# Optimization experiments

Measured on AMD Instinct MI355X. Metric: run time of the kernel, lower is better.

Reference implementation:

```python
import jax, jax.numpy as jnp
import numpy as np

B, S = 2, 2048
HID = 2560
NH, NKV, HD = 20, 5, 128
GROUPS = NH // NKV  # 4
THETA = 500000.0
RMS_EPS = 1e-6  # RMSNorm default eps used for attn_sub_norm
NEG_INF = -1e9


def pack_ternary(key, M, K):
    """Pack ternary weights {-1,0,1} (stored as trits {0,1,2}) into SIMD
    block-interleaved uint8 layout: per 128-elem block, byte j holds
    weights j+0 (bits 6:7), j+32 (4:5), j+64 (2:3), j+96 (0:1)."""
    t = jax.random.randint(key, (M, K), 0, 3).astype(jnp.uint8)
    t = t.reshape(M, K // 128, 4, 32)
    byte = (t[:, :, 0] << 6) | (t[:, :, 1] << 4) | (t[:, :, 2] << 2) | t[:, :, 3]
    return byte.reshape(M, K // 4)


def unpack_ternary(packed):
    """Inverse of pack_ternary -> float weights in {-1,0,1}. (M, K//4) -> (M, K)."""
    M, Kp = packed.shape
    nb = Kp // 32
    b = packed.reshape(M, nb, 32)
    fields = jnp.stack([(b >> 6) & 3, (b >> 4) & 3, (b >> 2) & 3, b & 3], axis=2)
    return fields.reshape(M, nb * 128).astype(jnp.float32) - 1.0


def bitlinear(x, packed, scale):
    w = unpack_ternary(packed) * scale  # (out, in)
    return jnp.einsum('bsi,oi->bso', x, w)


def rotate_half(x):
    h = x.shape[-1] // 2
    return jnp.concatenate([-x[..., h:], x[..., :h]], axis=-1)


def rms_norm(x, w, eps=RMS_EPS):
    var = jnp.mean(jnp.square(x.astype(jnp.float32)), axis=-1, keepdims=True)
    return (w * (x * jax.lax.rsqrt(var + eps))).astype(x.dtype)


def setup_inputs() -> dict:
    key = jax.random.key(0)
    ks = jax.random.split(key, 6)
    hidden_states = jax.random.normal(ks[0], (B, S, HID), dtype=jnp.float32)
    causal = jnp.tril(jnp.ones((S, S), dtype=bool))
    attention_mask = jnp.where(causal, 0.0, NEG_INF).astype(jnp.float32)[None, None]
    return {
        'hidden_states': hidden_states,
        'attention_mask': attention_mask,
        'q_w': pack_ternary(ks[1], NH * HD, HID),
        'k_w': pack_ternary(ks[2], NKV * HD, HID),
        'v_w': pack_ternary(ks[3], NKV * HD, HID),
        'o_w': pack_ternary(ks[4], HID, NH * HD),
        'q_scale': jnp.float32(0.02),
        'k_scale': jnp.float32(0.02),
        'v_scale': jnp.float32(0.02),
        'o_scale': jnp.float32(0.02),
        'attn_norm_w': jnp.ones((NH * HD,), dtype=jnp.float32),
    }


def reference(hidden_states, attention_mask, q_w, k_w, v_w, o_w,
              q_scale, k_scale, v_scale, o_scale, attn_norm_w):
    bsz, seq_len, _ = hidden_states.shape
    q = bitlinear(hidden_states, q_w, q_scale)
    k = bitlinear(hidden_states, k_w, k_scale)
    v = bitlinear(hidden_states, v_w, v_scale)
    q = q.reshape(bsz, seq_len, NH, HD).transpose(0, 2, 1, 3)    # (b,h,s,d)
    k = k.reshape(bsz, seq_len, NKV, HD).transpose(0, 2, 1, 3)
    v = v.reshape(bsz, seq_len, NKV, HD).transpose(0, 2, 1, 3)
    # rotary embedding
    inv_freq = 1.0 / (THETA ** (jnp.arange(0, HD, 2, dtype=jnp.float32) / HD))
    t = jnp.arange(seq_len, dtype=jnp.float32)
    freqs = t[:, None] * inv_freq[None, :]            # (s, d/2)
    emb = jnp.concatenate([freqs, freqs], axis=-1)    # (s, d)
    cos, sin = jnp.cos(emb), jnp.sin(emb)
    q = q * cos + rotate_half(q) * sin
    k = k * cos + rotate_half(k) * sin
    # GQA: repeat kv heads
    k = jnp.repeat(k, GROUPS, axis=1)
    v = jnp.repeat(v, GROUPS, axis=1)
    scores = jnp.einsum('bhqd,bhkd->bhqk', q, k) / np.sqrt(HD).astype(np.float32)
    scores = scores + attention_mask
    attn = jax.nn.softmax(scores.astype(jnp.float32), axis=-1).astype(q.dtype)
    out = jnp.einsum('bhqk,bhkd->bhqd', attn, v)
    out = out.transpose(0, 2, 1, 3).reshape(bsz, seq_len, NH * HD)
    out = rms_norm(out, attn_norm_w)
    return bitlinear(out, o_w, o_scale)
```

## Files before the change

### kernel.cpp

```cpp
#include <hip/hip_runtime.h>
#include <cstdint>
#include <cstddef>

typedef __bf16 bf16x8 __attribute__((ext_vector_type(8)));
typedef float  f32x4  __attribute__((ext_vector_type(4)));
typedef int    i32x4  __attribute__((ext_vector_type(4)));
typedef unsigned short u16x4 __attribute__((ext_vector_type(4)));

#define DEV __device__ __forceinline__
#define NEGINF (-__builtin_inff())

DEV uint16_t f2bf(float f) {
  union { float f; uint32_t u; } v; v.f = f;
  uint32_t u = v.u;
  u += 0x7FFFu + ((u >> 16) & 1u);
  return (uint16_t)(u >> 16);
}
DEV float bf2f(uint16_t h) {
  union { uint32_t u; float f; } v; v.u = ((uint32_t)h) << 16;
  return v.f;
}

DEV void gload_lds16(const void* g, void* l) {
  __builtin_amdgcn_global_load_lds(
      (const __attribute__((address_space(1))) void*)g,
      (__attribute__((address_space(3))) void*)l, 16, 0, 0);
}


__global__ void k_f32_to_bf16(const float* __restrict__ in, uint16_t* __restrict__ out, int n4) {
  int i = blockIdx.x * blockDim.x + threadIdx.x;
  if (i >= n4) return;
  f32x4 v = *(const f32x4*)(in + (size_t)i * 4);
  u16x4 o;
  o[0] = f2bf(v[0]); o[1] = f2bf(v[1]); o[2] = f2bf(v[2]); o[3] = f2bf(v[3]);
  *(u16x4*)(out + (size_t)i * 4) = o;
}

__global__ void k_unpack(const uint32_t* __restrict__ p, uint16_t* __restrict__ w, int total, int Kq) {
  int idx = blockIdx.x * blockDim.x + threadIdx.x;
  if (idx >= total) return;
  int row = idx / Kq, pc = idx - row * Kq;
  int blk = pc >> 5, j = pc & 31;
  uint32_t b = p[idx] & 0xFFu;
  size_t base = (size_t)row * (size_t)(Kq * 4) + (size_t)blk * 128 + j;
  w[base]      = f2bf((float)((b >> 6) & 3u) - 1.0f);
  w[base + 32] = f2bf((float)((b >> 4) & 3u) - 1.0f);
  w[base + 64] = f2bf((float)((b >> 2) & 3u) - 1.0f);
  w[base + 96] = f2bf((float)(b & 3u) - 1.0f);
}

__global__ void k_rope_table(float* __restrict__ cosT, float* __restrict__ sinT) {
  int idx = blockIdx.x * blockDim.x + threadIdx.x;
  int s = idx >> 6, i = idx & 63;
  float inv = expf((float)i * (-13.122363377404328f / 64.0f));
  float fr = (float)s * inv;
  cosT[idx] = cosf(fr);
  sinT[idx] = sinf(fr);
}

__global__ void k_rope(uint16_t* __restrict__ buf, const float* __restrict__ cosT,
                       const float* __restrict__ sinT, int H, int total) {
  int idx = blockIdx.x * blockDim.x + threadIdx.x;
  if (idx >= total) return;
  int d = idx & 63;
  int t = idx >> 6;
  int h = t % H;
  int row = t / H;
  int s = row & 2047;
  size_t base = (size_t)row * (size_t)(H * 128) + (size_t)h * 128 + d;
  float x1 = bf2f(buf[base]), x2 = bf2f(buf[base + 64]);
  float c = cosT[(s << 6) + d], sn = sinT[(s << 6) + d];
  buf[base]      = f2bf(x1 * c - x2 * sn);
  buf[base + 64] = f2bf(x2 * c + x1 * sn);
}

template<int MODE>
__global__ __launch_bounds__(256, 2)
void k_gemm(const uint16_t* __restrict__ A, const uint16_t* __restrict__ W,
            uint16_t* __restrict__ Qo, uint16_t* __restrict__ Ko, uint16_t* __restrict__ Vo,
            float* __restrict__ Fo,
            const float* __restrict__ s0p, const float* __restrict__ s1p, const float* __restrict__ s2p,
            int M, int N, int K)
{
  __shared__ uint16_t As[128 * 64];
  __shared__ uint16_t Bs[128 * 64];
  const int tid = threadIdx.x;
  const int n0 = blockIdx.x * 128, m0 = blockIdx.y * 128;
  const int lane = tid & 63, w = tid >> 6;
  const int wm = (w >> 1) * 64, wn = (w & 1) * 64;
  const int lr = lane & 15, lg = lane >> 4, lk = lg * 8;
  const size_t K2 = (size_t)K * 2;
  f32x4 acc[4][4] = {};

  const int srow = tid >> 3;
  const int cprime = ((tid & 7) * 16) ^ ((srow & 7) << 4);
  const uint8_t* Ag = (const uint8_t*)A + (size_t)(m0 + srow) * K2 + cprime;
  const uint8_t* Wg = (const uint8_t*)W + (size_t)(n0 + srow) * K2 + cprime;
  char* Al = (char*)As + w * 1024;
  char* Bl = (char*)Bs + w * 1024;

  for (size_t k0b = 0; k0b < K2; k0b += 128) {
    #pragma unroll
    for (int i = 0; i < 4; ++i)
      gload_lds16(Ag + (size_t)(i * 32) * K2 + k0b, Al + i * 4096);
    #pragma unroll
    for (int i = 0; i < 4; ++i)
      gload_lds16(Wg + (size_t)(i * 32) * K2 + k0b, Bl + i * 4096);
    __syncthreads();
    #pragma unroll
    for (int kc = 0; kc < 64; kc += 32) {
      bf16x8 a[4], b[4];
      #pragma unroll
      for (int i = 0; i < 4; ++i) {
        const int r = wm + i * 16 + lr;
        a[i] = *(const bf16x8*)((const char*)As + r * 128 + (((kc + lk) * 2) ^ ((r & 7) << 4)));
      }
      #pragma unroll
      for (int j = 0; j < 4; ++j) {
        const int r = wn + j * 16 + lr;
        b[j] = *(const bf16x8*)((const char*)Bs + r * 128 + (((kc + lk) * 2) ^ ((r & 7) << 4)));
      }
      #pragma unroll
      for (int i = 0; i < 4; ++i)
        #pragma unroll
        for (int j = 0; j < 4; ++j)
          acc[i][j] = __builtin_amdgcn_mfma_f32_16x16x32_bf16(a[i], b[j], acc[i][j], 0, 0, 0);
    }
    __syncthreads();
  }

  if (MODE == 0) {
    const float qs = *s0p, ks = *s1p, vs = *s2p;
    #pragma unroll
    for (int i = 0; i < 4; ++i) {
      const int rowb = m0 + wm + i * 16 + lg * 4;
      #pragma unroll
      for (int j = 0; j < 4; ++j) {
        const int col = n0 + wn + j * 16 + lr;
        #pragma unroll
        for (int r = 0; r < 4; ++r) {
          const int rr = rowb + r;
          const float v = acc[i][j][r];
          if (col < 2560) {
            Qo[(size_t)rr * 2560 + col] = f2bf(v * qs);
          } else if (col < 3200) {
            Ko[(size_t)rr * 640 + (col - 2560)] = f2bf(v * ks);
          } else {
            const int n2 = col - 3200;
            const int kvh = n2 >> 7, d = n2 & 127;
            const int bb = rr >> 11, ss = rr & 2047;
            Vo[(((size_t)(bb * 5 + kvh) * 128 + d) << 11) + ss] = f2bf(v * vs);
          }
        }
      }
    }
  } else {
    const float os = *s0p;
    #pragma unroll
    for (int i = 0; i < 4; ++i) {
      const int rowb = m0 + wm + i * 16 + lg * 4;
      #pragma unroll
      for (int j = 0; j < 4; ++j) {
        const int col = n0 + wn + j * 16 + lr;
        #pragma unroll
        for (int r = 0; r < 4; ++r)
          Fo[(size_t)(rowb + r) * N + col] = acc[i][j][r] * os;
      }
    }
  }
}

__global__ __launch_bounds__(256, 2)
void k_attn(const uint16_t* __restrict__ Q, const uint16_t* __restrict__ Kb,
            const uint16_t* __restrict__ Vt, uint16_t* __restrict__ Ob)
{
  __shared__ char Klds[2][16384];
  __shared__ char Vlds[2][16384];
  __shared__ uint16_t p_lds[4][16][72];

  const int lin = blockIdx.x;
  const int gslot = (lin & 7) * 80 + (lin >> 3);
  const int bk = gslot >> 6;
  const int st = 63 - (gslot & 63);
  const int b = bk / 5, kvh = bk - b * 5;

  const int tid = threadIdx.x, lane = tid & 63, w = tid >> 6;
  const int lr = lane & 15, lg = lane >> 4, lk = lg * 8;
  const int h = kvh * 4 + w;
  uint16_t (*pl)[72] = p_lds[w];
  const int kswz = (lr & 7) << 4;

  const uint8_t* Kg = (const uint8_t*)(Kb + (size_t)b * 2048 * 640 + (size_t)kvh * 128);
  const uint8_t* Vg = (const uint8_t*)(Vt + ((size_t)(b * 5 + kvh) * 128) * 2048);

  const int krow = tid >> 4;
  const int kcol = ((tid & 15) * 16) ^ ((krow & 7) << 4);
  const int vrow = tid >> 3;
  const int vcol = ((tid & 7) * 16) ^ ((vrow & 7) << 4);
  const int dst16 = tid * 16;

  const float C = 0.127531019577f;

  const int q0 = st * 32;
  const int ns = (q0 + 95) >> 6;

  bf16x8 qf0[4], qf1[4];
  {
    const size_t qb0 = ((size_t)(b * 2048 + q0 + lr)) * 2560 + (size_t)h * 128 + lk;
    #pragma unroll
    for (int c = 0; c < 4; ++c) {
      qf0[c] = *(const bf16x8*)&Q[qb0 + c * 32];
      qf1[c] = *(const bf16x8*)&Q[qb0 + 16 * 2560 + c * 32];
    }
  }

  {
    const uint8_t* Ks = Kg + (size_t)krow * 1280 + kcol;
    const uint8_t* Vs = Vg + (size_t)vrow * 4096 + vcol;
    #pragma unroll
    for (int i = 0; i < 4; ++i) gload_lds16(Ks + (size_t)i * 16 * 1280, Klds[0] + dst16 + i * 4096);
    #pragma unroll
    for (int i = 0; i < 4; ++i) gload_lds16(Vs + (size_t)i * 32 * 4096, Vlds[0] + dst16 + i * 4096);
  }

  int cur = 0;
  float m0 = NEGINF, m1 = NEGINF, l0 = 0.f, l1 = 0.f;
  f32x4 oa0[8] = {}, oa1[8] = {};

  #pragma unroll 1
  for (int stp = 0; stp < ns; ++stp) {
    const int k0 = stp * 64;
    __syncthreads();

    if (stp + 1 < ns) {
      const int kn = k0 + 64;
      const uint8_t* Ks = Kg + (size_t)(kn + krow) * 1280 + kcol;
      const uint8_t* Vs = Vg + (size_t)vrow * 4096 + (size_t)kn * 2 + vcol;
      char* Kd = Klds[cur ^ 1] + dst16;
      char* Vd = Vlds[cur ^ 1] + dst16;
      #pragma unroll
      for (int i = 0; i < 4; ++i) gload_lds16(Ks + (size_t)i * 16 * 1280, Kd + i * 4096);
      #pragma unroll
      for (int i = 0; i < 4; ++i) gload_lds16(Vs + (size_t)i * 32 * 4096, Vd + i * 4096);
    }

    const char* Kc = Klds[cur];
    const char* Vc = Vlds[cur];

    __builtin_amdgcn_s_setprio(1);
    f32x4 sa0[4] = {}, sa1[4] = {};
    #pragma unroll
    for (int t = 0; t < 4; ++t) {
      #pragma unroll
      for (int c = 0; c < 4; ++c) {
        bf16x8 kf = *(const bf16x8*)(Kc + (t * 16 + lr) * 256 + ((c * 64 + lg * 16) ^ kswz));
        sa0[t] = __builtin_amdgcn_mfma_f32_16x16x32_bf16(kf, qf0[c], sa0[t], 0, 0, 0);
        sa1[t] = __builtin_amdgcn_mfma_f32_16x16x32_bf16(kf, qf1[c], sa1[t], 0, 0, 0);
      }
    }
    __builtin_amdgcn_s_setprio(0);

    #pragma unroll
    for (int g = 0; g < 2; ++g) {
      const f32x4* sa = g ? sa1 : sa0;
      f32x4* oa = g ? oa1 : oa0;
      float& m = g ? m1 : m0;
      float& l = g ? l1 : l0;
      const int q0g = q0 + 16 * g;

      float u[16];
      if (k0 + 63 > q0g) {
        #pragma unroll
        for (int t = 0; t < 4; ++t)
          #pragma unroll
          for (int r = 0; r < 4; ++r)
            u[t * 4 + r] = (k0 + t * 16 + lg * 4 + r <= q0g + lr) ? sa[t][r] * C : NEGINF;
      } else {
        #pragma unroll
        for (int t = 0; t < 4; ++t)
          #pragma unroll
          for (int r = 0; r < 4; ++r)
            u[t * 4 + r] = sa[t][r] * C;
      }
      float m01 = fmaxf(u[0], u[1]),   m23 = fmaxf(u[2], u[3]);
      float m45 = fmaxf(u[4], u[5]),   m67 = fmaxf(u[6], u[7]);
      float m89 = fmaxf(u[8], u[9]),   mab = fmaxf(u[10], u[11]);
      float mcd = fmaxf(u[12], u[13]), mef = fmaxf(u[14], u[15]);
      float mx = fmaxf(fmaxf(fmaxf(m01, m23), fmaxf(m45, m67)),
                       fmaxf(fmaxf(m89, mab), fmaxf(mcd, mef)));
      mx = fmaxf(mx, __shfl_xor(mx, 16));
      mx = fmaxf(mx, __shfl_xor(mx, 32));
      const float mn = fmaxf(m, mx);
      const float resc = __builtin_exp2f(m - mn);
      m = mn;
      float pv[16];
      #pragma unroll
      for (int i = 0; i < 16; ++i) pv[i] = __builtin_exp2f(u[i] - mn);
      float s0 = (pv[0] + pv[1]) + (pv[2] + pv[3]);
      float s1 = (pv[4] + pv[5]) + (pv[6] + pv[7]);
      float s2 = (pv[8] + pv[9]) + (pv[10] + pv[11]);
      float s3 = (pv[12] + pv[13]) + (pv[14] + pv[15]);
      l = l * resc + ((s0 + s1) + (s2 + s3));
      #pragma unroll
      for (int t = 0; t < 4; ++t) {
        union { __bf16 b4[4]; unsigned long long u64; } pk;
        #pragma unroll
        for (int r = 0; r < 4; ++r) pk.b4[r] = (__bf16)pv[t * 4 + r];
        *(unsigned long long*)&pl[lr][t * 16 + lg * 4] = pk.u64;
      }
      #pragma unroll
      for (int dc = 0; dc < 8; ++dc) {
        oa[dc][0] *= resc; oa[dc][1] *= resc; oa[dc][2] *= resc; oa[dc][3] *= resc;
      }
      bf16x8 pa0 = *(const bf16x8*)&pl[lr][lk];
      bf16x8 pa1 = *(const bf16x8*)&pl[lr][32 + lk];
      __builtin_amdgcn_s_setprio(1);
      #pragma unroll
      for (int dc = 0; dc < 8; ++dc) {
        bf16x8 vf0 = *(const bf16x8*)(Vc + (dc * 16 + lr) * 128 + ((lg * 16) ^ kswz));
        bf16x8 vf1 = *(const bf16x8*)(Vc + (dc * 16 + lr) * 128 + ((64 + lg * 16) ^ kswz));
        oa[dc] = __builtin_amdgcn_mfma_f32_16x16x32_bf16(vf0, pa0, oa[dc], 0, 0, 0);
        oa[dc] = __builtin_amdgcn_mfma_f32_16x16x32_bf16(vf1, pa1, oa[dc], 0, 0, 0);
      }
      __builtin_amdgcn_s_setprio(0);
    }
    cur ^= 1;
  }

  #pragma unroll
  for (int g = 0; g < 2; ++g) {
    f32x4* oa = g ? oa1 : oa0;
    float lf = g ? l1 : l0;
    lf += __shfl_xor(lf, 16);
    lf += __shfl_xor(lf, 32);
    const float inv = 1.0f / lf;
    const size_t obase = ((size_t)(b * 2048 + q0 + 16 * g + lr)) * 2560 + (size_t)h * 128;
    #pragma unroll
    for (int dc = 0; dc < 8; ++dc) {
      union { __bf16 b4[4]; unsigned long long u64; } ok;
      #pragma unroll
      for (int r = 0; r < 4; ++r) ok.b4[r] = (__bf16)(oa[dc][r] * inv);
      *(unsigned long long*)&Ob[obase + dc * 16 + lg * 4] = ok.u64;
    }
  }
}

__global__ __launch_bounds__(256)
void k_rmsnorm(const uint16_t* __restrict__ X, const float* __restrict__ g, uint16_t* __restrict__ Y)
{
  const int row = blockIdx.x;
  const int tid = threadIdx.x;
  const uint16_t* x = X + (size_t)row * 2560;
  float ss = 0.f;
  #pragma unroll
  for (int it = 0; it < 10; ++it) {
    const int i = tid + it * 256;
    const float v = bf2f(x[i]);
    ss += v * v;
  }
  #pragma unroll
  for (int off = 1; off < 64; off <<= 1) ss += __shfl_xor(ss, off, 64);
  __shared__ float sred[4];
  if ((tid & 63) == 0) sred[tid >> 6] = ss;
  __syncthreads();
  const float tot = sred[0] + sred[1] + sred[2] + sred[3];
  const float rs = rsqrtf(tot * (1.0f / 2560.0f) + 1e-6f);
  uint16_t* y = Y + (size_t)row * 2560;
  #pragma unroll
  for (int it = 0; it < 10; ++it) {
    const int i = tid + it * 256;
    y[i] = f2bf(bf2f(x[i]) * rs * g[i]);
  }
}

extern "C" void kernel_launch(void* const* d_in, const int* in_sizes, int n_in,
                              void* d_out, int out_size, void* d_ws, size_t ws_size,
                              hipStream_t stream)
{
  const float*    x     = (const float*)d_in[0];
  const uint32_t* qw    = (const uint32_t*)d_in[2];
  const uint32_t* kw    = (const uint32_t*)d_in[3];
  const uint32_t* vw    = (const uint32_t*)d_in[4];
  const uint32_t* ow    = (const uint32_t*)d_in[5];
  const float*    qs    = (const float*)d_in[6];
  const float*    ks    = (const float*)d_in[7];
  const float*    vs    = (const float*)d_in[8];
  const float*    os    = (const float*)d_in[9];
  const float*    gnorm = (const float*)d_in[10];

  char* ws = (char*)d_ws;
  uint16_t* xb   = (uint16_t*)(ws + 0);
  uint16_t* wqkv = (uint16_t*)(ws + 20971520);
  uint16_t* owb  = (uint16_t*)(ws + 40632320);
  float*    cosT = (float*)   (ws + 53739520);
  float*    sinT = (float*)   (ws + 54263808);
  uint16_t* Qb   = (uint16_t*)(ws + 54788096);
  uint16_t* Kb   = (uint16_t*)(ws + 75759616);
  uint16_t* Vt   = (uint16_t*)(ws + 81002496);

  k_f32_to_bf16<<<10240, 256, 0, stream>>>(x, xb, 2621440);
  k_unpack<<<6400, 256, 0, stream>>>(qw, wqkv, 1638400, 640);
  k_unpack<<<1600, 256, 0, stream>>>(kw, wqkv + (size_t)2560 * 2560, 409600, 640);
  k_unpack<<<1600, 256, 0, stream>>>(vw, wqkv + (size_t)3200 * 2560, 409600, 640);
  k_unpack<<<6400, 256, 0, stream>>>(ow, owb, 1638400, 640);
  k_rope_table<<<512, 256, 0, stream>>>(cosT, sinT);

  k_gemm<0><<<dim3(30, 32), 256, 0, stream>>>(xb, wqkv, Qb, Kb, Vt, nullptr,
                                              qs, ks, vs, 4096, 3840, 2560);
  k_rope<<<20480, 256, 0, stream>>>(Qb, cosT, sinT, 20, 5242880);
  k_rope<<<5120, 256, 0, stream>>>(Kb, cosT, sinT, 5, 1310720);

  k_attn<<<dim3(640), 256, 0, stream>>>(Qb, Kb, Vt, xb);

  k_rmsnorm<<<4096, 256, 0, stream>>>(xb, gnorm, Qb);

  k_gemm<1><<<dim3(20, 32), 256, 0, stream>>>(Qb, owb, nullptr, nullptr, nullptr,
                                              (float*)d_out, os, nullptr, nullptr,
                                              4096, 2560, 2560);
}
```

Baseline: 316.2 us.

## Fuse Q rope into attention, fold RMSNorm into output GEMM, lazy softmax rescale

Merges the four weight-unpack launches into one kernel and folds the RMSNorm gain into the unpacked output-projection weights. The norm now only computes a per-row rsqrt, which the output GEMM applies in its epilogue. Q rotary embedding moves into the attention kernel's Q fragment load, removing a full pass over Q. The online softmax skips the max update and accumulator rescale unless the new max exceeds the old by a threshold. This trades extra per-fragment work in attention and some bf16 rounding differences for fewer memory passes.

New measurement: 297.3 us (median of 3 runs). 1.06x faster.

```diff
diff --git a/kernel.cpp b/kernel.cpp
--- a/kernel.cpp
+++ b/kernel.cpp
@@ -37,17 +37,35 @@
   *(u16x4*)(out + (size_t)i * 4) = o;
 }
 
-__global__ void k_unpack(const uint32_t* __restrict__ p, uint16_t* __restrict__ w, int total, int Kq) {
+__global__ void k_unpack_all(const uint32_t* __restrict__ qw, const uint32_t* __restrict__ kw,
+                             const uint32_t* __restrict__ vw, const uint32_t* __restrict__ ow,
+                             uint16_t* __restrict__ wqkv, uint16_t* __restrict__ owb,
+                             const float* __restrict__ g) {
   int idx = blockIdx.x * blockDim.x + threadIdx.x;
-  if (idx >= total) return;
-  int row = idx / Kq, pc = idx - row * Kq;
-  int blk = pc >> 5, j = pc & 31;
-  uint32_t b = p[idx] & 0xFFu;
-  size_t base = (size_t)row * (size_t)(Kq * 4) + (size_t)blk * 128 + j;
-  w[base]      = f2bf((float)((b >> 6) & 3u) - 1.0f);
-  w[base + 32] = f2bf((float)((b >> 4) & 3u) - 1.0f);
-  w[base + 64] = f2bf((float)((b >> 2) & 3u) - 1.0f);
-  w[base + 96] = f2bf((float)(b & 3u) - 1.0f);
+  if (idx >= 4096000) return;
+  if (idx < 2457600) {
+    int local = (idx < 1638400) ? idx : ((idx < 2048000) ? idx - 1638400 : idx - 2048000);
+    const uint32_t* s = (idx < 1638400) ? qw : ((idx < 2048000) ? kw : vw);
+    uint32_t b = s[local] & 0xFFu;
+    int drow = idx / 640, pc = idx - drow * 640;
+    int blk = pc >> 5, j = pc & 31;
+    size_t base = (size_t)drow * 2560 + (size_t)blk * 128 + j;
+    wqkv[base]      = f2bf((float)((b >> 6) & 3u) - 1.0f);
+    wqkv[base + 32] = f2bf((float)((b >> 4) & 3u) - 1.0f);
+    wqkv[base + 64] = f2bf((float)((b >> 2) & 3u) - 1.0f);
+    wqkv[base + 96] = f2bf((float)(b & 3u) - 1.0f);
+  } else {
+    int local = idx - 2457600;
+    uint32_t b = ow[local] & 0xFFu;
+    int drow = local / 640, pc = local - drow * 640;
+    int blk = pc >> 5, j = pc & 31;
+    int kpos = blk * 128 + j;
+    size_t base = (size_t)drow * 2560 + kpos;
+    owb[base]      = f2bf(((float)((b >> 6) & 3u) - 1.0f) * g[kpos]);
+    owb[base + 32] = f2bf(((float)((b >> 4) & 3u) - 1.0f) * g[kpos + 32]);
+    owb[base + 64] = f2bf(((float)((b >> 2) & 3u) - 1.0f) * g[kpos + 64]);
+    owb[base + 96] = f2bf(((float)(b & 3u) - 1.0f) * g[kpos + 96]);
+  }
 }
 
 __global__ void k_rope_table(float* __restrict__ cosT, float* __restrict__ sinT) {
@@ -165,7 +183,7 @@
         const int col = n0 + wn + j * 16 + lr;
         #pragma unroll
         for (int r = 0; r < 4; ++r)
-          Fo[(size_t)(rowb + r) * N + col] = acc[i][j][r] * os;
+          Fo[(size_t)(rowb + r) * N + col] = acc[i][j][r] * os * s1p[rowb + r];
       }
     }
   }
@@ -173,7 +191,8 @@
 
 __global__ __launch_bounds__(256, 2)
 void k_attn(const uint16_t* __restrict__ Q, const uint16_t* __restrict__ Kb,
-            const uint16_t* __restrict__ Vt, uint16_t* __restrict__ Ob)
+            const uint16_t* __restrict__ Vt, uint16_t* __restrict__ Ob,
+            const float* __restrict__ cosT, const float* __restrict__ sinT)
 {
   __shared__ char Klds[2][16384];
   __shared__ char Vlds[2][16384];
@@ -212,6 +231,28 @@
     for (int c = 0; c < 4; ++c) {
       qf0[c] = *(const bf16x8*)&Q[qb0 + c * 32];
       qf1[c] = *(const bf16x8*)&Q[qb0 + 16 * 2560 + c * 32];
+    }
+  }
+  #pragma unroll
+  for (int g = 0; g < 2; ++g) {
+    bf16x8* qf = g ? qf1 : qf0;
+    const int s = q0 + 16 * g + lr;
+    const int tb0 = s * 64 + lg * 8;
+    #pragma unroll
+    for (int c = 0; c < 2; ++c) {
+      const int tb = tb0 + c * 32;
+      f32x4 csa = *(const f32x4*)&cosT[tb];
+      f32x4 csb = *(const f32x4*)&cosT[tb + 4];
+      f32x4 sna = *(const f32x4*)&sinT[tb];
+      f32x4 snb = *(const f32x4*)&sinT[tb + 4];
+      #pragma unroll
+      for (int j = 0; j < 8; ++j) {
+        const float cs = (j < 4) ? csa[j] : csb[j - 4];
+        const float sn = (j < 4) ? sna[j] : snb[j - 4];
+        const float x1 = (float)qf[c][j], x2 = (float)qf[c + 2][j];
+        qf[c][j]     = (__bf16)(x1 * cs - x2 * sn);
+        qf[c + 2][j] = (__bf16)(x2 * cs + x1 * sn);
+      }
     }
   }
 
@@ -269,49 +310,54 @@
       float& l = g ? l1 : l0;
       const int q0g = q0 + 16 * g;
 
-      float u[16];
+      float sraw[16];
       if (k0 + 63 > q0g) {
         #pragma unroll
         for (int t = 0; t < 4; ++t)
           #pragma unroll
           for (int r = 0; r < 4; ++r)
-            u[t * 4 + r] = (k0 + t * 16 + lg * 4 + r <= q0g + lr) ? sa[t][r] * C : NEGINF;
+            sraw[t * 4 + r] = (k0 + t * 16 + lg * 4 + r <= q0g + lr) ? sa[t][r] : NEGINF;
       } else {
         #pragma unroll
         for (int t = 0; t < 4; ++t)
           #pragma unroll
           for (int r = 0; r < 4; ++r)
-            u[t * 4 + r] = sa[t][r] * C;
-      }
-      float m01 = fmaxf(u[0], u[1]),   m23 = fmaxf(u[2], u[3]);
-      float m45 = fmaxf(u[4], u[5]),   m67 = fmaxf(u[6], u[7]);
-      float m89 = fmaxf(u[8], u[9]),   mab = fmaxf(u[10], u[11]);
-      float mcd = fmaxf(u[12], u[13]), mef = fmaxf(u[14], u[15]);
-      float mx = fmaxf(fmaxf(fmaxf(m01, m23), fmaxf(m45, m67)),
-                       fmaxf(fmaxf(m89, mab), fmaxf(mcd, mef)));
-      mx = fmaxf(mx, __shfl_xor(mx, 16));
-      mx = fmaxf(mx, __shfl_xor(mx, 32));
-      const float mn = fmaxf(m, mx);
-      const float resc = __builtin_exp2f(m - mn);
-      m = mn;
+            sraw[t * 4 + r] = sa[t][r];
+      }
+      float a01 = fmaxf(sraw[0], sraw[1]),   a23 = fmaxf(sraw[2], sraw[3]);
+      float a45 = fmaxf(sraw[4], sraw[5]),   a67 = fmaxf(sraw[6], sraw[7]);
+      float a89 = fmaxf(sraw[8], sraw[9]),   aab = fmaxf(sraw[10], sraw[11]);
+      float acd = fmaxf(sraw[12], sraw[13]), aef = fmaxf(sraw[14], sraw[15]);
+      float mxr = fmaxf(fmaxf(fmaxf(a01, a23), fmaxf(a45, a67)),
+                        fmaxf(fmaxf(a89, aab), fmaxf(acd, aef)));
+      mxr = fmaxf(mxr, __shfl_xor(mxr, 16));
+      mxr = fmaxf(mxr, __shfl_xor(mxr, 32));
+      const float mx_u = mxr * C;
+      if (!__all(mx_u <= m + 8.0f)) {
+        const float mn = fmaxf(m, mx_u);
+        const float resc = __builtin_exp2f(m - mn);
+        m = mn;
+        l *= resc;
+        #pragma unroll
+        for (int dc = 0; dc < 8; ++dc) {
+          oa[dc][0] *= resc; oa[dc][1] *= resc; oa[dc][2] *= resc; oa[dc][3] *= resc;
+        }
+      }
+      const float nm = -m;
       float pv[16];
       #pragma unroll
-      for (int i = 0; i < 16; ++i) pv[i] = __builtin_exp2f(u[i] - mn);
+      for (int i = 0; i < 16; ++i) pv[i] = __builtin_exp2f(fmaf(sraw[i], C, nm));
       float s0 = (pv[0] + pv[1]) + (pv[2] + pv[3]);
       float s1 = (pv[4] + pv[5]) + (pv[6] + pv[7]);
       float s2 = (pv[8] + pv[9]) + (pv[10] + pv[11]);
       float s3 = (pv[12] + pv[13]) + (pv[14] + pv[15]);
-      l = l * resc + ((s0 + s1) + (s2 + s3));
+      l += (s0 + s1) + (s2 + s3);
       #pragma unroll
       for (int t = 0; t < 4; ++t) {
         union { __bf16 b4[4]; unsigned long long u64; } pk;
         #pragma unroll
         for (int r = 0; r < 4; ++r) pk.b4[r] = (__bf16)pv[t * 4 + r];
         *(unsigned long long*)&pl[lr][t * 16 + lg * 4] = pk.u64;
-      }
-      #pragma unroll
-      for (int dc = 0; dc < 8; ++dc) {
-        oa[dc][0] *= resc; oa[dc][1] *= resc; oa[dc][2] *= resc; oa[dc][3] *= resc;
       }
       bf16x8 pa0 = *(const bf16x8*)&pl[lr][lk];
       bf16x8 pa1 = *(const bf16x8*)&pl[lr][32 + lk];
@@ -347,7 +393,7 @@
 }
 
 __global__ __launch_bounds__(256)
-void k_rmsnorm(const uint16_t* __restrict__ X, const float* __restrict__ g, uint16_t* __restrict__ Y)
+void k_rowrms(const uint16_t* __restrict__ X, float* __restrict__ rs)
 {
   const int row = blockIdx.x;
   const int tid = threadIdx.x;
@@ -364,13 +410,9 @@
   __shared__ float sred[4];
   if ((tid & 63) == 0) sred[tid >> 6] = ss;
   __syncthreads();
-  const float tot = sred[0] + sred[1] + sred[2] + sred[3];
-  const float rs = rsqrtf(tot * (1.0f / 2560.0f) + 1e-6f);
-  uint16_t* y = Y + (size_t)row * 2560;
-  #pragma unroll
-  for (int it = 0; it < 10; ++it) {
-    const int i = tid + it * 256;
-    y[i] = f2bf(bf2f(x[i]) * rs * g[i]);
+  if (tid == 0) {
+    const float tot = sred[0] + sred[1] + sred[2] + sred[3];
+    rs[row] = rsqrtf(tot * (1.0f / 2560.0f) + 1e-6f);
   }
 }
 
@@ -398,24 +440,21 @@
   uint16_t* Qb   = (uint16_t*)(ws + 54788096);
   uint16_t* Kb   = (uint16_t*)(ws + 75759616);
   uint16_t* Vt   = (uint16_t*)(ws + 81002496);
+  float*    rsb  = (float*)   (ws + 54788096);
 
   k_f32_to_bf16<<<10240, 256, 0, stream>>>(x, xb, 2621440);
-  k_unpack<<<6400, 256, 0, stream>>>(qw, wqkv, 1638400, 640);
-  k_unpack<<<1600, 256, 0, stream>>>(kw, wqkv + (size_t)2560 * 2560, 409600, 640);
-  k_unpack<<<1600, 256, 0, stream>>>(vw, wqkv + (size_t)3200 * 2560, 409600, 640);
-  k_unpack<<<6400, 256, 0, stream>>>(ow, owb, 1638400, 640);
+  k_unpack_all<<<16000, 256, 0, stream>>>(qw, kw, vw, ow, wqkv, owb, gnorm);
   k_rope_table<<<512, 256, 0, stream>>>(cosT, sinT);
 
   k_gemm<0><<<dim3(30, 32), 256, 0, stream>>>(xb, wqkv, Qb, Kb, Vt, nullptr,
                                               qs, ks, vs, 4096, 3840, 2560);
-  k_rope<<<20480, 256, 0, stream>>>(Qb, cosT, sinT, 20, 5242880);
   k_rope<<<5120, 256, 0, stream>>>(Kb, cosT, sinT, 5, 1310720);
 
-  k_attn<<<dim3(640), 256, 0, stream>>>(Qb, Kb, Vt, xb);
-
-  k_rmsnorm<<<4096, 256, 0, stream>>>(xb, gnorm, Qb);
-
-  k_gemm<1><<<dim3(20, 32), 256, 0, stream>>>(Qb, owb, nullptr, nullptr, nullptr,
-                                              (float*)d_out, os, nullptr, nullptr,
+  k_attn<<<dim3(640), 256, 0, stream>>>(Qb, Kb, Vt, xb, cosT, sinT);
+
+  k_rowrms<<<4096, 256, 0, stream>>>(xb, rsb);
+
+  k_gemm<1><<<dim3(20, 32), 256, 0, stream>>>(xb, owb, nullptr, nullptr, nullptr,
+                                              (float*)d_out, os, rsb, nullptr,
                                               4096, 2560, 2560);
 }
```
